# Performance work log

Hardware: AMD Instinct MI355X
Metric: run time of the kernel (lower is better)

## Reference

```python
import jax, jax.numpy as jnp
import numpy as np

L, P = 8, 512
HID = 128
N_COARSE, N_FINE = 64, 128
LVIS_NEAR, LVIS_FAR = 1e-3, 0.5
S = 100.0  # 1 / fixed_s_recp


def _mlp_sdf(x, w0, b0, w1, b1, w2, b2, w3, b3):
    # x: [..., 3] -> sdf [...]
    h = jax.nn.relu(x @ w0 + b0)
    h = jax.nn.relu(h @ w1 + b1)
    h = jax.nn.relu(h @ w2 + b2)
    return (h @ w3 + b3)[..., 0]


def _sdf_to_w(sdf, s):
    # faithful to sdf_to_w: cdf -> alpha -> visibility weights via cumprod
    cdf = jax.nn.sigmoid(sdf * s)
    alpha = jnp.clip((cdf[..., :-1] - cdf[..., 1:]) / (cdf[..., :-1] + 1e-10), 0.0, None)
    ones = jnp.ones(alpha.shape[:-1] + (1,), alpha.dtype)
    shifted = jnp.concatenate([ones, 1.0 - alpha + 1e-10], axis=-1)
    return alpha * jnp.cumprod(shifted, axis=-1)[..., :-1]


def _sample_pdf(bins, weights, u):
    # standard NeRF importance sampling; bins [...,M+1], weights [...,M], u [...,N]
    weights = weights + 1e-5
    pdf = weights / jnp.sum(weights, axis=-1, keepdims=True)
    cdf = jnp.cumsum(pdf, axis=-1)
    cdf = jnp.concatenate([jnp.zeros_like(cdf[..., :1]), cdf], axis=-1)  # [...,M+1]
    # searchsorted (right) via broadcast compare: [...,N,M+1]
    inds = jnp.sum((u[..., None] >= cdf[..., None, :]).astype(jnp.int32), axis=-1)
    below = jnp.clip(inds - 1, 0, cdf.shape[-1] - 1)
    above = jnp.clip(inds, 0, cdf.shape[-1] - 1)
    cdf_b = jnp.take_along_axis(cdf, below, axis=-1)
    cdf_a = jnp.take_along_axis(cdf, above, axis=-1)
    bins_b = jnp.take_along_axis(bins, below, axis=-1)
    bins_a = jnp.take_along_axis(bins, above, axis=-1)
    denom = cdf_a - cdf_b
    denom = jnp.where(denom < 1e-5, jnp.ones_like(denom), denom)
    t = (u - cdf_b) / denom
    return bins_b + t * (bins_a - bins_b)


def setup_inputs() -> dict:
    key = jax.random.key(0)
    ks = jax.random.split(key, 8)

    def lin(k, fi, fo):
        return jax.random.normal(k, (fi, fo), jnp.float32) / jnp.sqrt(jnp.float32(fi))

    return {
        "pts": jax.random.normal(ks[0], (1, P, 3), jnp.float32) * 0.5,
        "light_posi": jax.random.normal(ks[1], (L, 3), jnp.float32) * 2.0,
        "u": jax.random.uniform(ks[2], (L, P, N_FINE), jnp.float32),
        "w0": lin(ks[3], 3, HID), "b0": jnp.zeros((HID,), jnp.float32),
        "w1": lin(ks[4], HID, HID), "b1": jnp.zeros((HID,), jnp.float32),
        "w2": lin(ks[5], HID, HID), "b2": jnp.zeros((HID,), jnp.float32),
        "w3": lin(ks[6], HID, 1), "b3": jnp.zeros((1,), jnp.float32),
    }


def reference(pts, light_posi, u, w0, b0, w1, b1, w2, b2, w3, b3):
    sdf = lambda x: _mlp_sdf(x, w0, b0, w1, b1, w2, b2, w3, b3)
    # pts: [1,P,3]; light_posi: [L,3]
    pts2l = light_posi[:, None, :] - pts  # [L,P,3]
    pts2l = pts2l / jnp.linalg.norm(pts2l, axis=-1, keepdims=True)
    t = jnp.linspace(0.0, 1.0 - 1.0 / N_COARSE, N_COARSE, dtype=jnp.float32)
    d_coarse = LVIS_NEAR * (1.0 - t) + LVIS_FAR * t  # [N_COARSE]
    d_coarse = jnp.broadcast_to(d_coarse, (pts2l.shape[0], pts.shape[1], N_COARSE))
    # coarse sample points: [L,P,Nc,3]
    pts_coarse = pts[:, :, None, :] + d_coarse[..., None] * pts2l[:, :, None, :]
    w_coarse = _sdf_to_w(sdf(pts_coarse), S)  # [L,P,Nc-1]
    d_fine = _sample_pdf(d_coarse, w_coarse, u)  # [L,P,Nf]
    d_all = jnp.sort(jnp.concatenate([d_coarse, d_fine], axis=-1), axis=-1)  # [L,P,Nc+Nf]
    pts_all = pts[:, :, None, :] + d_all[..., None] * pts2l[:, :, None, :]
    w_all = _sdf_to_w(sdf(pts_all), S)
    occu = jnp.sum(w_all, axis=-1)  # [L,P]
    return 1.0 - occu
```

## Files before the change

### kernel.cpp

```cpp
#include <hip/hip_runtime.h>
#include <math.h>

#define NL 8
#define NP 512
#define NC 64
#define NF 128
#define NALL 192
#define NRAY (NL * NP)
#define HID 128

typedef _Float16 half8 __attribute__((ext_vector_type(8)));
typedef _Float16 half4v __attribute__((ext_vector_type(4)));
typedef float floatx16 __attribute__((ext_vector_type(16)));
typedef unsigned long long ull;

#define MFMA(a, b, c) __builtin_amdgcn_mfma_f32_32x32x16_f16((a), (b), (c), 0, 0, 0)


__device__ __forceinline__ float dcoarse_at(int i) {
    float t = (float)i * 0.015625f;
    return 1e-3f * (1.0f - t) + 0.5f * t;
}

__device__ __forceinline__ floatx16 fzero16() {
    floatx16 z;
#pragma unroll
    for (int i = 0; i < 16; ++i) z[i] = 0.f;
    return z;
}
__device__ __forceinline__ half8 hzero8() {
    half8 z;
#pragma unroll
    for (int i = 0; i < 8; ++i) z[i] = (_Float16)0.f;
    return z;
}

__global__ void prep_kernel(const float* __restrict__ w1, const float* __restrict__ w2,
                            _Float16* __restrict__ Wsp) {
    int f = blockIdx.x * 256 + threadIdx.x;
    int layer = blockIdx.y;
    const float* w = layer ? w2 : w1;
    int i = f & 7, l31 = (f >> 3) & 31, lhi = (f >> 8) & 1, ks = (f >> 9) & 7, jb = f >> 12;
    int j = jb * 32 + l31;
    int k = ks * 16 + lhi * 8 + i;
    float v = w[k * 128 + j];
    _Float16 hi = (_Float16)v;
    Wsp[(layer * 2 + 0) * 16384 + f] = hi;
    Wsp[(layer * 2 + 1) * 16384 + f] = (_Float16)(v - (float)hi);
}

template<int MODE, int FASTW>
__global__ __launch_bounds__(256, 2) void mlp_kernel(
    const float* __restrict__ pts, const float* __restrict__ lights,
    const float* __restrict__ d_fine,
    const float* __restrict__ w0, const float* __restrict__ b0,
    const float* __restrict__ w1, const float* __restrict__ b1,
    const float* __restrict__ w2, const float* __restrict__ b2,
    const float* __restrict__ w3, const float* __restrict__ b3,
    const _Float16* __restrict__ Wsp,
    float* __restrict__ sdf_out)
{
    __shared__ __align__(16) _Float16 Hhi[128 * 128];
    __shared__ __align__(16) _Float16 Hlo[128 * 128];
    __shared__ _Float16 Xs[6 * 128];
    __shared__ float P2[2 * 128];

    const int tid = threadIdx.x;
    const int lane = tid & 63;
    const int wv = tid >> 6;
    const int jh = wv & 1, mh = wv >> 1;
    const int l31 = lane & 31, lhi = lane >> 5;
    const int base = blockIdx.x * 128;

    if (tid < 128) {
        int pt = base + tid;
        int ray; float d;
        if (MODE == 0) { ray = pt >> 6; d = dcoarse_at(pt & 63); }
        else           { ray = pt >> 7; d = d_fine[pt]; }
        int l = ray >> 9, p = ray & (NP - 1);
        float px = pts[p * 3 + 0], py = pts[p * 3 + 1], pz = pts[p * 3 + 2];
        float dx = lights[l * 3 + 0] - px, dy = lights[l * 3 + 1] - py, dz = lights[l * 3 + 2] - pz;
        float n = sqrtf(dx * dx + dy * dy + dz * dz);
        dx /= n; dy /= n; dz /= n;
        float xc[3] = { px + d * dx, py + d * dy, pz + d * dz };
#pragma unroll
        for (int c = 0; c < 3; ++c) {
            _Float16 h = (_Float16)xc[c];
            Xs[c * 128 + tid] = h;
            Xs[(3 + c) * 128 + tid] = (_Float16)(xc[c] - (float)h);
        }
    }
    __syncthreads();

    const int m0 = mh * 64;

    auto haddr = [&](int m, int k0) {
        return m * 128 + ((((k0 >> 3) ^ (m & 15)) << 3) | (k0 & 7));
    };

    auto store_tile = [&](const floatx16& a, int jt, int mt, const float* __restrict__ bias) {
        int m = m0 + mt * 32 + l31;
#pragma unroll
        for (int g = 0; g < 4; ++g) {
            int jg = jh * 64 + jt * 32 + 8 * g + 4 * lhi;
            half4v hq, lq;
#pragma unroll
            for (int q = 0; q < 4; ++q) {
                float v = fmaxf(a[g * 4 + q] + bias[jg + q], 0.f);
                _Float16 hi = (_Float16)v;
                hq[q] = hi;
                lq[q] = (_Float16)(v - (float)hi);
            }
            int ad = haddr(m, jg);
            *(half4v*)&Hhi[ad] = hq;
            *(half4v*)&Hlo[ad] = lq;
        }
    };

    floatx16 acc[2][2];

    {
        half8 a1h[2], a1l[2], bh1[2], bl1[2];
#pragma unroll
        for (int jt = 0; jt < 2; ++jt) { a1h[jt] = hzero8(); a1l[jt] = hzero8(); }
#pragma unroll
        for (int mt = 0; mt < 2; ++mt) { bh1[mt] = hzero8(); bl1[mt] = hzero8(); }
        if (lhi == 0) {
#pragma unroll
            for (int jt = 0; jt < 2; ++jt) {
                int j = jh * 64 + jt * 32 + l31;
#pragma unroll
                for (int c = 0; c < 3; ++c) {
                    float v = w0[c * 128 + j];
                    _Float16 hi = (_Float16)v;
                    a1h[jt][c] = hi;
                    a1l[jt][c] = (_Float16)(v - (float)hi);
                }
            }
#pragma unroll
            for (int mt = 0; mt < 2; ++mt) {
                int m = m0 + mt * 32 + l31;
#pragma unroll
                for (int c = 0; c < 3; ++c) {
                    bh1[mt][c] = Xs[c * 128 + m];
                    bl1[mt][c] = Xs[(3 + c) * 128 + m];
                }
            }
        }
#pragma unroll
        for (int jt = 0; jt < 2; ++jt)
#pragma unroll
            for (int mt = 0; mt < 2; ++mt) acc[jt][mt] = fzero16();
#pragma unroll
        for (int jt = 0; jt < 2; ++jt)
#pragma unroll
            for (int mt = 0; mt < 2; ++mt) acc[jt][mt] = MFMA(a1l[jt], bh1[mt], acc[jt][mt]);
#pragma unroll
        for (int jt = 0; jt < 2; ++jt)
#pragma unroll
            for (int mt = 0; mt < 2; ++mt) acc[jt][mt] = MFMA(a1h[jt], bl1[mt], acc[jt][mt]);
#pragma unroll
        for (int jt = 0; jt < 2; ++jt)
#pragma unroll
            for (int mt = 0; mt < 2; ++mt) acc[jt][mt] = MFMA(a1h[jt], bh1[mt], acc[jt][mt]);
#pragma unroll
        for (int jt = 0; jt < 2; ++jt)
#pragma unroll
            for (int mt = 0; mt < 2; ++mt) store_tile(acc[jt][mt], jt, mt, b0);
    }
    __syncthreads();

    auto ldA = [&](int L, int jt, int ks, half8& ah, half8& al) {
        if (FASTW) {
            int off = ((((jh * 2 + jt) * 8 + ks) * 2 + lhi) * 32 + l31) * 8;
            ah = *(const half8*)&Wsp[(L * 2 + 0) * 16384 + off];
            al = *(const half8*)&Wsp[(L * 2 + 1) * 16384 + off];
        } else {
            const float* w = L ? w2 : w1;
            int j = jh * 64 + jt * 32 + l31, k0 = ks * 16 + lhi * 8;
#pragma unroll
            for (int i = 0; i < 8; ++i) {
                float v = w[(k0 + i) * 128 + j];
                _Float16 hi = (_Float16)v;
                ah[i] = hi;
                al[i] = (_Float16)(v - (float)hi);
            }
        }
    };

    half8 bh[2][8], bl[2][8];

    auto gemm = [&](int L) {
#pragma unroll
        for (int mt = 0; mt < 2; ++mt) {
            int m = m0 + mt * 32 + l31;
#pragma unroll
            for (int ks = 0; ks < 8; ++ks) {
                int ad = haddr(m, ks * 16 + lhi * 8);
                bh[mt][ks] = *(const half8*)&Hhi[ad];
                bl[mt][ks] = *(const half8*)&Hlo[ad];
            }
        }
#pragma unroll
        for (int jt = 0; jt < 2; ++jt)
#pragma unroll
            for (int mt = 0; mt < 2; ++mt) acc[jt][mt] = fzero16();
#pragma unroll
        for (int ks = 0; ks < 8; ++ks) {
            half8 ah[2], al[2];
            ldA(L, 0, ks, ah[0], al[0]);
            ldA(L, 1, ks, ah[1], al[1]);
#pragma unroll
            for (int jt = 0; jt < 2; ++jt)
#pragma unroll
                for (int mt = 0; mt < 2; ++mt) acc[jt][mt] = MFMA(al[jt], bh[mt][ks], acc[jt][mt]);
#pragma unroll
            for (int jt = 0; jt < 2; ++jt)
#pragma unroll
                for (int mt = 0; mt < 2; ++mt) acc[jt][mt] = MFMA(ah[jt], bl[mt][ks], acc[jt][mt]);
#pragma unroll
            for (int jt = 0; jt < 2; ++jt)
#pragma unroll
                for (int mt = 0; mt < 2; ++mt) acc[jt][mt] = MFMA(ah[jt], bh[mt][ks], acc[jt][mt]);
        }
    };

    gemm(0);
    __syncthreads();
#pragma unroll
    for (int jt = 0; jt < 2; ++jt)
#pragma unroll
        for (int mt = 0; mt < 2; ++mt) store_tile(acc[jt][mt], jt, mt, b1);
    __syncthreads();

    gemm(1);
#pragma unroll
    for (int mt = 0; mt < 2; ++mt) {
        float p = 0.f;
#pragma unroll
        for (int jt = 0; jt < 2; ++jt)
#pragma unroll
            for (int g = 0; g < 4; ++g) {
                int jg = jh * 64 + jt * 32 + 8 * g + 4 * lhi;
#pragma unroll
                for (int q = 0; q < 4; ++q) {
                    float v = fmaxf(acc[jt][mt][g * 4 + q] + b2[jg + q], 0.f);
                    p = fmaf(v, w3[jg + q], p);
                }
            }
        p += __shfl_xor(p, 32);
        if (lane < 32) P2[jh * 128 + m0 + mt * 32 + l31] = p;
    }
    __syncthreads();
    if (tid < 128) sdf_out[base + tid] = b3[0] + P2[tid] + P2[128 + tid];
}

__global__ __launch_bounds__(256) void sample_kernel(
    const float* __restrict__ sdf_c, const float* __restrict__ u,
    float* __restrict__ d_fine, unsigned char* __restrict__ perm8) {
    const int lane = threadIdx.x & 63, wv = threadIdx.x >> 6;
    const int ray = blockIdx.x * 4 + wv;

    float sv = sdf_c[ray * NC + lane];
    float c = 1.0f / (1.0f + expf(-100.0f * sv));
    float cn = __shfl_down(c, 1);
    bool valid = lane < 63;
    float a = valid ? fmaxf((c - cn) / (c + 1e-10f), 0.f) : 0.f;
    float sh = valid ? (1.f - a + 1e-10f) : 1.f;
    float ps = sh;
#pragma unroll
    for (int off = 1; off < 64; off <<= 1) { float o = __shfl_up(ps, off); if (lane >= off) ps *= o; }
    float T = __shfl_up(ps, 1);
    if (lane == 0) T = 1.f;
    float w = valid ? (a * T + 1e-5f) : 0.f;
    float wsum = w;
#pragma unroll
    for (int off = 1; off < 64; off <<= 1) wsum += __shfl_xor(wsum, off);
    float pdf = w / wsum;
    float cs = pdf;
#pragma unroll
    for (int off = 1; off < 64; off <<= 1) { float o = __shfl_up(cs, off); if (lane >= off) cs += o; }
    float cdfv = __shfl_up(cs, 1);
    if (lane == 0) cdfv = 0.f;

    float df[2];
#pragma unroll
    for (int t = 0; t < 2; ++t) {
        float uu = u[ray * NF + t * 64 + lane];
        int lo = 0;
#pragma unroll
        for (int b = 32; b >= 1; b >>= 1) {
            float cm = __shfl(cdfv, lo + b);
            if (uu >= cm) lo += b;
        }
        int above = min(lo + 1, NC - 1);
        float cb = __shfl(cdfv, lo), ca = __shfl(cdfv, above);
        float bb = dcoarse_at(lo), ba = dcoarse_at(above);
        float denom = ca - cb;
        if (denom < 1e-5f) denom = 1.f;
        float tt = (uu - cb) / denom;
        df[t] = bb + tt * (ba - bb);
        d_fine[ray * 128 + t * 64 + lane] = df[t];
    }

    ull v[4];
    v[0] = ((ull)__float_as_uint(dcoarse_at(lane)) << 32) | (unsigned)lane;
    v[1] = ((ull)__float_as_uint(df[0]) << 32) | (unsigned)(64 + lane);
    v[2] = ((ull)__float_as_uint(df[1]) << 32) | (unsigned)(128 + lane);
    v[3] = ((ull)0x7F800000u << 32) | 255u;
    for (int k = 2; k <= 256; k <<= 1) {
        for (int j = k >> 1; j > 0; j >>= 1) {
            if (j >= 64) {
                int tj = j >> 6;
#pragma unroll
                for (int t = 0; t < 4; ++t) {
                    if ((t & tj) == 0) {
                        int t2 = t ^ tj;
                        bool asc = (((t * 64) & k) == 0);
                        ull x = v[t], y = v[t2];
                        bool sw = asc ? (x > y) : (x < y);
                        if (sw) { v[t] = y; v[t2] = x; }
                    }
                }
            } else {
#pragma unroll
                for (int t = 0; t < 4; ++t) {
                    int i = t * 64 + lane;
                    ull other = __shfl_xor(v[t], j);
                    bool lower = (lane & j) == 0;
                    bool asc = ((i & k) == 0);
                    bool takeMin = (lower == asc);
                    ull mn = v[t] < other ? v[t] : other;
                    ull mx = v[t] < other ? other : v[t];
                    v[t] = takeMin ? mn : mx;
                }
            }
        }
    }
#pragma unroll
    for (int t = 0; t < 3; ++t)
        perm8[ray * NALL + t * 64 + lane] = (unsigned char)(v[t] & 0xFFu);
}

__global__ __launch_bounds__(256) void finish_kernel(
    const float* __restrict__ sdf_c, const float* __restrict__ sdf_f,
    const unsigned char* __restrict__ perm8, float* __restrict__ out) {
    int lane = threadIdx.x & 63, wv = threadIdx.x >> 6;
    int ray = blockIdx.x * 4 + wv;
    const unsigned char* P = perm8 + (size_t)ray * NALL;
    float c[4];
#pragma unroll
    for (int t = 0; t < 4; ++t) {
        int i = lane * 3 + t;
        if (i < NALL) {
            int idx = P[i];
            float s = (idx < 64) ? sdf_c[ray * NC + idx] : sdf_f[ray * 128 + (idx - 64)];
            c[t] = 1.0f / (1.0f + expf(-100.0f * s));
        } else c[t] = 0.f;
    }
    float a[3], s[3];
#pragma unroll
    for (int t = 0; t < 3; ++t) {
        int i = lane * 3 + t;
        if (i < NALL - 1) {
            a[t] = fmaxf((c[t] - c[t + 1]) / (c[t] + 1e-10f), 0.f);
            s[t] = 1.f - a[t] + 1e-10f;
        } else { a[t] = 0.f; s[t] = 1.f; }
    }
    float chunk = s[0] * s[1] * s[2];
    float ps = chunk;
#pragma unroll
    for (int off = 1; off < 64; off <<= 1) {
        float o = __shfl_up(ps, off);
        if (lane >= off) ps *= o;
    }
    float T = __shfl_up(ps, 1);
    if (lane == 0) T = 1.f;
    float occ = a[0] * T;
    T *= s[0]; occ = fmaf(a[1], T, occ);
    T *= s[1]; occ = fmaf(a[2], T, occ);
#pragma unroll
    for (int off = 1; off < 64; off <<= 1) occ += __shfl_xor(occ, off);
    if (lane == 0) out[ray] = 1.f - occ;
}

extern "C" void kernel_launch(void* const* d_in, const int* in_sizes, int n_in,
                              void* d_out, int out_size, void* d_ws, size_t ws_size,
                              hipStream_t stream) {
    const float* pts = (const float*)d_in[0];
    const float* lights = (const float*)d_in[1];
    const float* u = (const float*)d_in[2];
    const float* w0 = (const float*)d_in[3];
    const float* b0 = (const float*)d_in[4];
    const float* w1 = (const float*)d_in[5];
    const float* b1 = (const float*)d_in[6];
    const float* w2 = (const float*)d_in[7];
    const float* b2 = (const float*)d_in[8];
    const float* w3 = (const float*)d_in[9];
    const float* b3 = (const float*)d_in[10];
    float* out = (float*)d_out;

    char* wsb = (char*)d_ws;
    float* sdf_c = (float*)wsb;
    float* sdf_f = (float*)(wsb + (size_t)NRAY * NC * 4);
    float* d_fine = (float*)(wsb + (size_t)NRAY * (NC + 128) * 4);
    unsigned char* perm8 = (unsigned char*)(wsb + (size_t)NRAY * (NC + 256) * 4);
    _Float16* Wsp = (_Float16*)(wsb + (size_t)NRAY * (NC + 256) * 4 + (size_t)NRAY * NALL);
    const size_t need = (size_t)NRAY * (NC + 256) * 4 + (size_t)NRAY * NALL
                      + (size_t)4 * 16384 * sizeof(_Float16);
    const bool fast = ws_size >= need;

    if (fast) {
        prep_kernel<<<dim3(64, 2), 256, 0, stream>>>(w1, w2, Wsp);
        mlp_kernel<0, 1><<<(NRAY * NC) / 128, 256, 0, stream>>>(
            pts, lights, nullptr, w0, b0, w1, b1, w2, b2, w3, b3, Wsp, sdf_c);
        sample_kernel<<<NRAY / 4, 256, 0, stream>>>(sdf_c, u, d_fine, perm8);
        mlp_kernel<1, 1><<<(NRAY * 128) / 128, 256, 0, stream>>>(
            pts, lights, d_fine, w0, b0, w1, b1, w2, b2, w3, b3, Wsp, sdf_f);
    } else {
        mlp_kernel<0, 0><<<(NRAY * NC) / 128, 256, 0, stream>>>(
            pts, lights, nullptr, w0, b0, w1, b1, w2, b2, w3, b3, nullptr, sdf_c);
        sample_kernel<<<NRAY / 4, 256, 0, stream>>>(sdf_c, u, d_fine, perm8);
        mlp_kernel<1, 0><<<(NRAY * 128) / 128, 256, 0, stream>>>(
            pts, lights, d_fine, w0, b0, w1, b1, w2, b2, w3, b3, nullptr, sdf_f);
    }
    finish_kernel<<<NRAY / 4, 256, 0, stream>>>(sdf_c, sdf_f, perm8, out);
}
```

Measured before the change: 248.0 us.

## Halve MLP block tile to 64 points and raise occupancy to 4 blocks

Each MLP block now processes 64 sample points instead of 128, with one 32-row M tile per wave instead of two. This halves the shared memory per block and drops the preloaded B-fragment register arrays, and launch bounds now ask for 4 blocks per CU. The aim is more resident waves to hide latency and a smaller register footprint. In exchange, each A-weight fragment loaded from global memory feeds half as many MFMAs, so weight traffic per point doubles and twice as many blocks run.

```diff
diff --git a/kernel.cpp b/kernel.cpp
--- a/kernel.cpp
+++ b/kernel.cpp
@@ -50,7 +50,7 @@
 }
 
 template<int MODE, int FASTW>
-__global__ __launch_bounds__(256, 2) void mlp_kernel(
+__global__ __launch_bounds__(256, 4) void mlp_kernel(
     const float* __restrict__ pts, const float* __restrict__ lights,
     const float* __restrict__ d_fine,
     const float* __restrict__ w0, const float* __restrict__ b0,
@@ -60,19 +60,19 @@
     const _Float16* __restrict__ Wsp,
     float* __restrict__ sdf_out)
 {
-    __shared__ __align__(16) _Float16 Hhi[128 * 128];
-    __shared__ __align__(16) _Float16 Hlo[128 * 128];
-    __shared__ _Float16 Xs[6 * 128];
-    __shared__ float P2[2 * 128];
+    __shared__ __align__(16) _Float16 Hhi[64 * 128];
+    __shared__ __align__(16) _Float16 Hlo[64 * 128];
+    __shared__ _Float16 Xs[6 * 64];
+    __shared__ float P2[2 * 64];
 
     const int tid = threadIdx.x;
     const int lane = tid & 63;
     const int wv = tid >> 6;
     const int jh = wv & 1, mh = wv >> 1;
     const int l31 = lane & 31, lhi = lane >> 5;
-    const int base = blockIdx.x * 128;
-
-    if (tid < 128) {
+    const int base = blockIdx.x * 64;
+
+    if (tid < 64) {
         int pt = base + tid;
         int ray; float d;
         if (MODE == 0) { ray = pt >> 6; d = dcoarse_at(pt & 63); }
@@ -86,20 +86,20 @@
 #pragma unroll
         for (int c = 0; c < 3; ++c) {
             _Float16 h = (_Float16)xc[c];
-            Xs[c * 128 + tid] = h;
-            Xs[(3 + c) * 128 + tid] = (_Float16)(xc[c] - (float)h);
-        }
-    }
-    __syncthreads();
-
-    const int m0 = mh * 64;
+            Xs[c * 64 + tid] = h;
+            Xs[(3 + c) * 64 + tid] = (_Float16)(xc[c] - (float)h);
+        }
+    }
+    __syncthreads();
+
+    const int m0 = mh * 32;
 
     auto haddr = [&](int m, int k0) {
         return m * 128 + ((((k0 >> 3) ^ (m & 15)) << 3) | (k0 & 7));
     };
 
-    auto store_tile = [&](const floatx16& a, int jt, int mt, const float* __restrict__ bias) {
-        int m = m0 + mt * 32 + l31;
+    auto store_tile = [&](const floatx16& a, int jt, const float* __restrict__ bias) {
+        int m = m0 + l31;
 #pragma unroll
         for (int g = 0; g < 4; ++g) {
             int jg = jh * 64 + jt * 32 + 8 * g + 4 * lhi;
@@ -117,14 +117,13 @@
         }
     };
 
-    floatx16 acc[2][2];
+    floatx16 acc[2];
 
     {
-        half8 a1h[2], a1l[2], bh1[2], bl1[2];
+        half8 a1h[2], a1l[2], bh1, bl1;
 #pragma unroll
         for (int jt = 0; jt < 2; ++jt) { a1h[jt] = hzero8(); a1l[jt] = hzero8(); }
-#pragma unroll
-        for (int mt = 0; mt < 2; ++mt) { bh1[mt] = hzero8(); bl1[mt] = hzero8(); }
+        bh1 = hzero8(); bl1 = hzero8();
         if (lhi == 0) {
 #pragma unroll
             for (int jt = 0; jt < 2; ++jt) {
@@ -137,36 +136,23 @@
                     a1l[jt][c] = (_Float16)(v - (float)hi);
                 }
             }
-#pragma unroll
-            for (int mt = 0; mt < 2; ++mt) {
-                int m = m0 + mt * 32 + l31;
-#pragma unroll
-                for (int c = 0; c < 3; ++c) {
-                    bh1[mt][c] = Xs[c * 128 + m];
-                    bl1[mt][c] = Xs[(3 + c) * 128 + m];
-                }
-            }
-        }
-#pragma unroll
-        for (int jt = 0; jt < 2; ++jt)
-#pragma unroll
-            for (int mt = 0; mt < 2; ++mt) acc[jt][mt] = fzero16();
-#pragma unroll
-        for (int jt = 0; jt < 2; ++jt)
-#pragma unroll
-            for (int mt = 0; mt < 2; ++mt) acc[jt][mt] = MFMA(a1l[jt], bh1[mt], acc[jt][mt]);
-#pragma unroll
-        for (int jt = 0; jt < 2; ++jt)
-#pragma unroll
-            for (int mt = 0; mt < 2; ++mt) acc[jt][mt] = MFMA(a1h[jt], bl1[mt], acc[jt][mt]);
-#pragma unroll
-        for (int jt = 0; jt < 2; ++jt)
-#pragma unroll
-            for (int mt = 0; mt < 2; ++mt) acc[jt][mt] = MFMA(a1h[jt], bh1[mt], acc[jt][mt]);
-#pragma unroll
-        for (int jt = 0; jt < 2; ++jt)
-#pragma unroll
-            for (int mt = 0; mt < 2; ++mt) store_tile(acc[jt][mt], jt, mt, b0);
+            int m = m0 + l31;
+#pragma unroll
+            for (int c = 0; c < 3; ++c) {
+                bh1[c] = Xs[c * 64 + m];
+                bl1[c] = Xs[(3 + c) * 64 + m];
+            }
+        }
+#pragma unroll
+        for (int jt = 0; jt < 2; ++jt) acc[jt] = fzero16();
+#pragma unroll
+        for (int jt = 0; jt < 2; ++jt) acc[jt] = MFMA(a1l[jt], bh1, acc[jt]);
+#pragma unroll
+        for (int jt = 0; jt < 2; ++jt) acc[jt] = MFMA(a1h[jt], bl1, acc[jt]);
+#pragma unroll
+        for (int jt = 0; jt < 2; ++jt) acc[jt] = MFMA(a1h[jt], bh1, acc[jt]);
+#pragma unroll
+        for (int jt = 0; jt < 2; ++jt) store_tile(acc[jt], jt, b0);
     }
     __syncthreads();
 
@@ -188,54 +174,35 @@
         }
     };
 
-    half8 bh[2][8], bl[2][8];
-
     auto gemm = [&](int L) {
-#pragma unroll
-        for (int mt = 0; mt < 2; ++mt) {
-            int m = m0 + mt * 32 + l31;
-#pragma unroll
-            for (int ks = 0; ks < 8; ++ks) {
-                int ad = haddr(m, ks * 16 + lhi * 8);
-                bh[mt][ks] = *(const half8*)&Hhi[ad];
-                bl[mt][ks] = *(const half8*)&Hlo[ad];
-            }
-        }
-#pragma unroll
-        for (int jt = 0; jt < 2; ++jt)
-#pragma unroll
-            for (int mt = 0; mt < 2; ++mt) acc[jt][mt] = fzero16();
+        const int m = m0 + l31;
+#pragma unroll
+        for (int jt = 0; jt < 2; ++jt) acc[jt] = fzero16();
 #pragma unroll
         for (int ks = 0; ks < 8; ++ks) {
+            int ad = haddr(m, ks * 16 + lhi * 8);
+            half8 bh = *(const half8*)&Hhi[ad];
+            half8 bl = *(const half8*)&Hlo[ad];
             half8 ah[2], al[2];
             ldA(L, 0, ks, ah[0], al[0]);
             ldA(L, 1, ks, ah[1], al[1]);
-#pragma unroll
-            for (int jt = 0; jt < 2; ++jt)
-#pragma unroll
-                for (int mt = 0; mt < 2; ++mt) acc[jt][mt] = MFMA(al[jt], bh[mt][ks], acc[jt][mt]);
-#pragma unroll
-            for (int jt = 0; jt < 2; ++jt)
-#pragma unroll
-                for (int mt = 0; mt < 2; ++mt) acc[jt][mt] = MFMA(ah[jt], bl[mt][ks], acc[jt][mt]);
-#pragma unroll
-            for (int jt = 0; jt < 2; ++jt)
-#pragma unroll
-                for (int mt = 0; mt < 2; ++mt) acc[jt][mt] = MFMA(ah[jt], bh[mt][ks], acc[jt][mt]);
+            acc[0] = MFMA(al[0], bh, acc[0]);
+            acc[1] = MFMA(al[1], bh, acc[1]);
+            acc[0] = MFMA(ah[0], bl, acc[0]);
+            acc[1] = MFMA(ah[1], bl, acc[1]);
+            acc[0] = MFMA(ah[0], bh, acc[0]);
+            acc[1] = MFMA(ah[1], bh, acc[1]);
         }
     };
 
     gemm(0);
     __syncthreads();
 #pragma unroll
-    for (int jt = 0; jt < 2; ++jt)
-#pragma unroll
-        for (int mt = 0; mt < 2; ++mt) store_tile(acc[jt][mt], jt, mt, b1);
+    for (int jt = 0; jt < 2; ++jt) store_tile(acc[jt], jt, b1);
     __syncthreads();
 
     gemm(1);
-#pragma unroll
-    for (int mt = 0; mt < 2; ++mt) {
+    {
         float p = 0.f;
 #pragma unroll
         for (int jt = 0; jt < 2; ++jt)
@@ -244,15 +211,15 @@
                 int jg = jh * 64 + jt * 32 + 8 * g + 4 * lhi;
 #pragma unroll
                 for (int q = 0; q < 4; ++q) {
-                    float v = fmaxf(acc[jt][mt][g * 4 + q] + b2[jg + q], 0.f);
+                    float v = fmaxf(acc[jt][g * 4 + q] + b2[jg + q], 0.f);
                     p = fmaf(v, w3[jg + q], p);
                 }
             }
         p += __shfl_xor(p, 32);
-        if (lane < 32) P2[jh * 128 + m0 + mt * 32 + l31] = p;
-    }
-    __syncthreads();
-    if (tid < 128) sdf_out[base + tid] = b3[0] + P2[tid] + P2[128 + tid];
+        if (lane < 32) P2[jh * 64 + m0 + l31] = p;
+    }
+    __syncthreads();
+    if (tid < 64) sdf_out[base + tid] = b3[0] + P2[tid] + P2[64 + tid];
 }
 
 __global__ __launch_bounds__(256) void sample_kernel(
@@ -412,16 +379,16 @@
 
     if (fast) {
         prep_kernel<<<dim3(64, 2), 256, 0, stream>>>(w1, w2, Wsp);
-        mlp_kernel<0, 1><<<(NRAY * NC) / 128, 256, 0, stream>>>(
+        mlp_kernel<0, 1><<<(NRAY * NC) / 64, 256, 0, stream>>>(
             pts, lights, nullptr, w0, b0, w1, b1, w2, b2, w3, b3, Wsp, sdf_c);
         sample_kernel<<<NRAY / 4, 256, 0, stream>>>(sdf_c, u, d_fine, perm8);
-        mlp_kernel<1, 1><<<(NRAY * 128) / 128, 256, 0, stream>>>(
+        mlp_kernel<1, 1><<<(NRAY * 128) / 64, 256, 0, stream>>>(
             pts, lights, d_fine, w0, b0, w1, b1, w2, b2, w3, b3, Wsp, sdf_f);
     } else {
-        mlp_kernel<0, 0><<<(NRAY * NC) / 128, 256, 0, stream>>>(
+        mlp_kernel<0, 0><<<(NRAY * NC) / 64, 256, 0, stream>>>(
             pts, lights, nullptr, w0, b0, w1, b1, w2, b2, w3, b3, nullptr, sdf_c);
         sample_kernel<<<NRAY / 4, 256, 0, stream>>>(sdf_c, u, d_fine, perm8);
-        mlp_kernel<1, 0><<<(NRAY * 128) / 128, 256, 0, stream>>>(
+        mlp_kernel<1, 0><<<(NRAY * 128) / 64, 256, 0, stream>>>(
             pts, lights, d_fine, w0, b0, w1, b1, w2, b2, w3, b3, nullptr, sdf_f);
     }
     finish_kernel<<<NRAY / 4, 256, 0, stream>>>(sdf_c, sdf_f, perm8, out);
```

After: 276.3 us. 1.11x slower.
